# Performance work log

Measured on AMD Instinct MI355X. Metric: run time of the kernel, lower is better.

## Reference

```python
import jax, jax.numpy as jnp
import numpy as np


def setup_inputs() -> dict:
    key = jax.random.key(0)
    k1, k2 = jax.random.split(key)
    B, C, M, N = 4, 3, 4096, 8192
    query = jax.random.normal(k1, (B, C, M), dtype=jnp.float32)
    points = jax.random.normal(k2, (B, C, N), dtype=jnp.float32)
    return {"k": 16, "query": query, "points": points}


def reference(k, query, points):
    # query: BxCxM, points: BxCxN  (trans=True path of original module)
    q = jnp.swapaxes(query, 1, 2)   # BxMxC
    p = jnp.swapaxes(points, 1, 2)  # BxNxC
    # squared L2 distances (FAISS GpuIndexFlatL2): BxMxN
    q2 = jnp.sum(q * q, axis=-1, keepdims=True)           # BxMx1
    p2 = jnp.sum(p * p, axis=-1)[:, None, :]              # Bx1xN
    dist = q2 + p2 - 2.0 * jnp.einsum('bmc,bnc->bmn', q, p)
    # k smallest distances, sorted ascending (FAISS sorts results)
    _, index_batch = jax.lax.top_k(-dist, k)              # BxMxK int32
    index_batch = index_batch.astype(jnp.int64) if index_batch.dtype != jnp.int64 else index_batch
    # gather neighbor coordinates: points BxCxN, idx BxMxK -> BxCxMxK
    neighbor_points = jax.vmap(lambda pts, idx: pts[:, idx])(points, index_batch)
    return neighbor_points, index_batch
```

## Files before the change

### kernel.cpp

```cpp
#include <hip/hip_runtime.h>
#include <stdint.h>

#define BQ 4
#define CC 3
#define MM 4096
#define NN 8192
#define KK 16
#define NP_OFF (BQ*CC*MM*KK)
#define BLOCK 256
#define RPW 8
#define ROWS 8
#define CHUNK 512
#define NCH 16
#define SCH 8
#define QST 2
#define EPSD 1e-4f
#define CANDMAX 128

__device__ __forceinline__ float rfl(float x) {
    return __uint_as_float((unsigned)__builtin_amdgcn_readfirstlane((int)__float_as_uint(x)));
}
__device__ __forceinline__ unsigned mapf(float f) {
    unsigned u = __float_as_uint(f);
    return (u & 0x80000000u) ? ~u : (u | 0x80000000u);
}
__device__ __forceinline__ float unmapf(unsigned u) {
    unsigned b = (u & 0x80000000u) ? (u & 0x7fffffffu) : ~u;
    return __uint_as_float(b);
}

__global__ __launch_bounds__(256) void prep_kernel(
    const float* __restrict__ points, float4* __restrict__ ws4)
{
    int i = blockIdx.x * 256 + threadIdx.x;
    int b = i >> 13, n = i & (NN - 1);
    const float* pb = points + b * (CC * NN);
    float px = pb[n], py = pb[NN + n], pz = pb[2*NN + n];
    float p2 = __fadd_rn(__fadd_rn(__fmul_rn(px,px), __fmul_rn(py,py)),
                         __fmul_rn(pz,pz));
    ws4[i] = make_float4(px, py, pz, -0.5f * p2);
}

__global__ __launch_bounds__(BLOCK, 8) void knn_kernel(
    const float* __restrict__ query,
    const float4* __restrict__ ws4,
    float* __restrict__ out)
{
    __shared__ float4 pts[2][CHUNK];
    __shared__ unsigned aux[ROWS][64];
    __shared__ unsigned scnt[ROWS];
    __shared__ unsigned rcbits[ROWS];

    const int tid  = threadIdx.x;
    const int lane = tid & 63;
    const int wv   = tid >> 6;
    const int bid  = blockIdx.x;
    const int b    = bid >> 9;
    const int rb   = (bid & 511) * ROWS;

    const float*  qb  = query + b * (CC * MM);
    const float4* wsb = ws4 + b * NN;

    ((unsigned*)aux)[tid]       = 0u;
    ((unsigned*)aux)[tid + 256] = 0u;
    if (tid < ROWS) scnt[tid] = 0u;

    float qx[RPW], qy[RPW], qz[RPW], dm[RPW];
    #pragma unroll
    for (int r = 0; r < RPW; ++r) {
        int m = rb + r;
        qx[r] = rfl(qb[m]);
        qy[r] = rfl(qb[MM + m]);
        qz[r] = rfl(qb[2*MM + m]);
        dm[r] = -__builtin_inff();
    }

    auto stage = [&](int ch, int bi) {
        pts[bi][tid]       = wsb[(ch << 9) + tid];
        pts[bi][256 + tid] = wsb[(ch << 9) + 256 + tid];
    };

    auto comp1 = [&](int bi) {
        #pragma unroll
        for (int t = 0; t < QST; ++t) {
            float4 P = pts[bi][((wv * QST + t) << 6) + lane];
            #pragma unroll
            for (int r = 0; r < RPW; ++r) {
                float dotf = __builtin_fmaf(qz[r], P.z,
                              __builtin_fmaf(qy[r], P.y,
                               __builtin_fmaf(qx[r], P.x, P.w)));
                dm[r] = fmaxf(dm[r], dotf);
            }
        }
    };

    stage(0, 0);
    #pragma unroll 1
    for (int ch = 0; ch < SCH; ch += 2) {
        __syncthreads();
        if (ch + 1 < SCH) stage(ch + 1, 1);
        comp1(0);
        __syncthreads();
        if (ch + 2 < SCH) stage(ch + 2, 0);
        if (ch + 1 < SCH) comp1(1);
    }

    #pragma unroll
    for (int r = 0; r < RPW; ++r)
        atomicMax(&aux[r][lane], mapf(dm[r]));
    __syncthreads();

    #pragma unroll
    for (int rr = 0; rr < 2; ++rr) {
        int row = 2*wv + rr;
        unsigned v = aux[row][lane];
        #pragma unroll
        for (int k = 2; k <= 64; k <<= 1) {
            #pragma unroll
            for (int j = k >> 1; j > 0; j >>= 1) {
                unsigned o = __shfl_xor(v, j, 64);
                bool keepmin = (((lane & j) == 0) == ((lane & k) == 0));
                v = keepmin ? (v < o ? v : o) : (v > o ? v : o);
            }
        }
        unsigned tb = __shfl(v, 48, 64);
        if (lane == 0) rcbits[row] = __float_as_uint(unmapf(tb) - EPSD);
    }
    __syncthreads();

    float rc[RPW];
    #pragma unroll
    for (int r = 0; r < RPW; ++r)
        rc[r] = rfl(__uint_as_float(rcbits[r]));

    unsigned short* cbase = (unsigned short*)&aux[0][0];
    auto comp2 = [&](int ch, int bi) {
        #pragma unroll
        for (int t = 0; t < QST; ++t) {
            int st = wv * QST + t;
            float4 P = pts[bi][(st << 6) + lane];
            unsigned n = (unsigned)((ch << 9) + (st << 6) + lane);
            #pragma unroll
            for (int r = 0; r < RPW; ++r) {
                float dotf = __builtin_fmaf(qz[r], P.z,
                              __builtin_fmaf(qy[r], P.y,
                               __builtin_fmaf(qx[r], P.x, P.w)));
                if (dotf >= rc[r]) {
                    unsigned pos = atomicAdd(&scnt[r], 1u);
                    if (pos < CANDMAX)
                        cbase[r * CANDMAX + pos] = (unsigned short)n;
                }
            }
        }
    };

    comp2(6, 0);
    comp2(7, 1);
    __syncthreads();
    stage(0, 0);
    #pragma unroll 1
    for (int i = 0; i < 14; i += 2) {
        int c0 = (i     < 6) ? i     : i + 2;
        int c1 = (i + 1 < 6) ? i + 1 : i + 3;
        int c2 = (i + 2 < 6) ? i + 2 : i + 4;
        __syncthreads();
        if (i + 1 < 14) stage(c1, 1);
        comp2(c0, 0);
        __syncthreads();
        if (i + 2 < 14) stage(c2, 0);
        if (i + 1 < 14) comp2(c1, 1);
    }
    __syncthreads();

    #pragma unroll
    for (int rr = 0; rr < 2; ++rr) {
        int row = 2*wv + rr;
        int m   = rb + row;
        float ex = rfl(qb[m]);
        float ey = rfl(qb[MM + m]);
        float ez = rfl(qb[2*MM + m]);
        float eq2 = rfl(__fadd_rn(__fadd_rn(__fmul_rn(ex,ex), __fmul_rn(ey,ey)),
                                  __fmul_rn(ez,ez)));
        unsigned c = scnt[row]; if (c > CANDMAX) c = CANDMAX;
        const unsigned short* c16 = cbase + row * CANDMAX;

        unsigned kb0 = ~0u, id0 = ~0u, kb1 = ~0u, id1 = ~0u;
        if (lane < (int)c) {
            id0 = c16[lane];
            float4 P = wsb[id0];
            float p2  = __fmul_rn(-2.0f, P.w);
            float dot = __builtin_fmaf(ez, P.z,
                         __builtin_fmaf(ey, P.y, __fmul_rn(ex, P.x)));
            kb0 = mapf(__fsub_rn(__fadd_rn(eq2, p2), __fmul_rn(2.0f, dot)));
        }
        if (64 + lane < (int)c) {
            id1 = c16[64 + lane];
            float4 P = wsb[id1];
            float p2  = __fmul_rn(-2.0f, P.w);
            float dot = __builtin_fmaf(ez, P.z,
                         __builtin_fmaf(ey, P.y, __fmul_rn(ex, P.x)));
            kb1 = mapf(__fsub_rn(__fadd_rn(eq2, p2), __fmul_rn(2.0f, dot)));
        }

        auto bsort = [&](unsigned& kb, unsigned& id) {
            #pragma unroll
            for (int k = 2; k <= 64; k <<= 1) {
                #pragma unroll
                for (int j = k >> 1; j > 0; j >>= 1) {
                    unsigned ok = __shfl_xor(kb, j, 64);
                    unsigned oi = __shfl_xor(id, j, 64);
                    bool takeMin  = (((lane & j) == 0) == ((lane & k) == 0));
                    bool selfLess = (kb < ok) || (kb == ok && id < oi);
                    if (selfLess != takeMin) { kb = ok; id = oi; }
                }
            }
        };
        bsort(kb0, id0);
        bsort(kb1, id1);
        unsigned rk = __shfl(kb1, 63 - lane, 64);
        unsigned ri = __shfl(id1, 63 - lane, 64);
        bool pLess = (rk < kb0) || (rk == kb0 && ri < id0);
        if (pLess) { kb0 = rk; id0 = ri; }
        #pragma unroll
        for (int j = 32; j > 0; j >>= 1) {
            unsigned ok = __shfl_xor(kb0, j, 64);
            unsigned oi = __shfl_xor(id0, j, 64);
            bool selfLess = (kb0 < ok) || (kb0 == ok && id0 < oi);
            bool takeMin  = ((lane & j) == 0);
            if (selfLess != takeMin) { kb0 = ok; id0 = oi; }
        }

        if (lane < KK) {
            int oi = (int)id0;
            float4 P = wsb[oi];
            out[NP_OFF + (b * MM + m) * KK + lane] = (float)oi;
            out[((b * CC + 0) * MM + m) * KK + lane] = P.x;
            out[((b * CC + 1) * MM + m) * KK + lane] = P.y;
            out[((b * CC + 2) * MM + m) * KK + lane] = P.z;
        }
    }
}

extern "C" void kernel_launch(void* const* d_in, const int* in_sizes, int n_in,
                              void* d_out, int out_size, void* d_ws, size_t ws_size,
                              hipStream_t stream) {
    const float* query  = (const float*)d_in[1];
    const float* points = (const float*)d_in[2];
    float4* ws4 = (float4*)d_ws;
    float* out = (float*)d_out;
    prep_kernel<<<dim3((BQ*NN)/256), dim3(256), 0, stream>>>(points, ws4);
    dim3 grid(BQ * (MM / ROWS));
    dim3 block(BLOCK);
    knn_kernel<<<grid, block, 0, stream>>>(query, ws4, out);
}
```

Baseline: 115.1 us.

## Replace LDS double-buffered point staging with direct per-wave global loads

Removes the shared-memory point buffers and the staged, barrier-synchronised chunk loops. Each wave now reads its own contiguous slice of point records straight from global memory (cache-resident) in both passes, and pass 2 scans all points in one flat loop instead of reusing chunks 6–7 from pass 1. This cuts LDS traffic and the many __syncthreads, and the smaller LDS footprint may raise occupancy. The cost is that each wave issues its own global loads with no sharing across the block, so speed now depends on L1/L2 hit rates and load latency hiding.

```diff
diff --git a/kernel.cpp b/kernel.cpp
--- a/kernel.cpp
+++ b/kernel.cpp
@@ -10,12 +10,10 @@
 #define BLOCK 256
 #define RPW 8
 #define ROWS 8
-#define CHUNK 512
-#define NCH 16
-#define SCH 8
-#define QST 2
 #define EPSD 1e-4f
 #define CANDMAX 128
+#define P1STEPS 16
+#define P2STEPS 32
 
 __device__ __forceinline__ float rfl(float x) {
     return __uint_as_float((unsigned)__builtin_amdgcn_readfirstlane((int)__float_as_uint(x)));
@@ -46,7 +44,6 @@
     const float4* __restrict__ ws4,
     float* __restrict__ out)
 {
-    __shared__ float4 pts[2][CHUNK];
     __shared__ unsigned aux[ROWS][64];
     __shared__ unsigned scnt[ROWS];
     __shared__ unsigned rcbits[ROWS];
@@ -74,35 +71,19 @@
         qz[r] = rfl(qb[2*MM + m]);
         dm[r] = -__builtin_inff();
     }
-
-    auto stage = [&](int ch, int bi) {
-        pts[bi][tid]       = wsb[(ch << 9) + tid];
-        pts[bi][256 + tid] = wsb[(ch << 9) + 256 + tid];
-    };
-
-    auto comp1 = [&](int bi) {
-        #pragma unroll
-        for (int t = 0; t < QST; ++t) {
-            float4 P = pts[bi][((wv * QST + t) << 6) + lane];
-            #pragma unroll
-            for (int r = 0; r < RPW; ++r) {
-                float dotf = __builtin_fmaf(qz[r], P.z,
-                              __builtin_fmaf(qy[r], P.y,
-                               __builtin_fmaf(qx[r], P.x, P.w)));
-                dm[r] = fmaxf(dm[r], dotf);
-            }
-        }
-    };
-
-    stage(0, 0);
-    #pragma unroll 1
-    for (int ch = 0; ch < SCH; ch += 2) {
-        __syncthreads();
-        if (ch + 1 < SCH) stage(ch + 1, 1);
-        comp1(0);
-        __syncthreads();
-        if (ch + 2 < SCH) stage(ch + 2, 0);
-        if (ch + 1 < SCH) comp1(1);
+    __syncthreads();
+
+    const float4* base1 = wsb + wv * (P1STEPS * 64);
+    #pragma unroll 4
+    for (int t = 0; t < P1STEPS; ++t) {
+        float4 P = base1[t * 64 + lane];
+        #pragma unroll
+        for (int r = 0; r < RPW; ++r) {
+            float dotf = __builtin_fmaf(qz[r], P.z,
+                          __builtin_fmaf(qy[r], P.y,
+                           __builtin_fmaf(qx[r], P.x, P.w)));
+            dm[r] = fmaxf(dm[r], dotf);
+        }
     }
 
     #pragma unroll
@@ -134,41 +115,23 @@
         rc[r] = rfl(__uint_as_float(rcbits[r]));
 
     unsigned short* cbase = (unsigned short*)&aux[0][0];
-    auto comp2 = [&](int ch, int bi) {
-        #pragma unroll
-        for (int t = 0; t < QST; ++t) {
-            int st = wv * QST + t;
-            float4 P = pts[bi][(st << 6) + lane];
-            unsigned n = (unsigned)((ch << 9) + (st << 6) + lane);
-            #pragma unroll
-            for (int r = 0; r < RPW; ++r) {
-                float dotf = __builtin_fmaf(qz[r], P.z,
-                              __builtin_fmaf(qy[r], P.y,
-                               __builtin_fmaf(qx[r], P.x, P.w)));
-                if (dotf >= rc[r]) {
-                    unsigned pos = atomicAdd(&scnt[r], 1u);
-                    if (pos < CANDMAX)
-                        cbase[r * CANDMAX + pos] = (unsigned short)n;
-                }
+    const unsigned nb2 = (unsigned)(wv * (P2STEPS * 64));
+    const float4* base2 = wsb + nb2;
+    #pragma unroll 4
+    for (int t = 0; t < P2STEPS; ++t) {
+        float4 P = base2[t * 64 + lane];
+        unsigned n = nb2 + (unsigned)(t * 64 + lane);
+        #pragma unroll
+        for (int r = 0; r < RPW; ++r) {
+            float dotf = __builtin_fmaf(qz[r], P.z,
+                          __builtin_fmaf(qy[r], P.y,
+                           __builtin_fmaf(qx[r], P.x, P.w)));
+            if (dotf >= rc[r]) {
+                unsigned pos = atomicAdd(&scnt[r], 1u);
+                if (pos < CANDMAX)
+                    cbase[r * CANDMAX + pos] = (unsigned short)n;
             }
         }
-    };
-
-    comp2(6, 0);
-    comp2(7, 1);
-    __syncthreads();
-    stage(0, 0);
-    #pragma unroll 1
-    for (int i = 0; i < 14; i += 2) {
-        int c0 = (i     < 6) ? i     : i + 2;
-        int c1 = (i + 1 < 6) ? i + 1 : i + 3;
-        int c2 = (i + 2 < 6) ? i + 2 : i + 4;
-        __syncthreads();
-        if (i + 1 < 14) stage(c1, 1);
-        comp2(c0, 0);
-        __syncthreads();
-        if (i + 2 < 14) stage(c2, 0);
-        if (i + 1 < 14) comp2(c1, 1);
     }
     __syncthreads();
 
```

New measurement: 108.6 us. 1.06x faster.
